# Kernel tuning notes

Measured on AMD Instinct MI355X. Metric: run time of the kernel, lower is better.

## Reference

```python
import jax, jax.numpy as jnp
import numpy as np

D_MODEL = 256
NHEAD = 8
HEAD_DIM = D_MODEL // NHEAD
NLAYERS = 8
LAYER_NAMES = ('self', 'cross', 'self', 'cross', 'self', 'cross', 'self', 'cross')
LN_EPS = 1e-5
ATTN_EPS = 1e-6


def _layernorm(x, g, b):
    mu = jnp.mean(x, axis=-1, keepdims=True)
    var = jnp.mean(jnp.square(x - mu), axis=-1, keepdims=True)
    return (x - mu) * jax.lax.rsqrt(var + LN_EPS) * g + b


def _encoder_layer(x, source, Wq, Wk, Wv, Wm, W1, W2, g1, b1, g2, b2):
    # x: [N, L, C], source: [N, S, C]; weights stored [in, out] so y = x @ W
    bs, L, C = x.shape
    S = source.shape[1]
    q = (x @ Wq).reshape(bs, L, NHEAD, HEAD_DIM)
    k = (source @ Wk).reshape(bs, S, NHEAD, HEAD_DIM)
    v = (source @ Wv).reshape(bs, S, NHEAD, HEAD_DIM)
    # LoFTR LinearAttention: feature map elu(x)+1, O(N d^2) kernelized attention
    Q = jax.nn.elu(q) + 1.0
    K = jax.nn.elu(k) + 1.0
    v_n = v / S  # normalize values by kv length for numerical stability
    KV = jnp.einsum('nshd,nshv->nhdv', K, v_n)            # [N,H,D,D]
    Z = 1.0 / (jnp.einsum('nlhd,nhd->nlh', Q, K.sum(axis=1)) + ATTN_EPS)
    msg = jnp.einsum('nlhd,nhdv,nlh->nlhv', Q, KV, Z) * S  # [N,L,H,D]
    msg = msg.reshape(bs, L, C) @ Wm
    msg = _layernorm(msg, g1, b1)
    h = jnp.concatenate([x, msg], axis=-1)                 # [N,L,2C]
    h = jax.nn.relu(h @ W1) @ W2
    h = _layernorm(h, g2, b2)
    return x + h


def _transformer(feat0, feat1, Wq, Wk, Wv, Wm, W1, W2, g1, b1, g2, b2):
    for i, name in enumerate(LAYER_NAMES):
        p = (Wq[i], Wk[i], Wv[i], Wm[i], W1[i], W2[i], g1[i], b1[i], g2[i], b2[i])
        if name == 'self':
            feat0 = _encoder_layer(feat0, feat0, *p)
            feat1 = _encoder_layer(feat1, feat1, *p)
        else:  # cross
            new0 = _encoder_layer(feat0, feat1, *p)
            feat1 = _encoder_layer(feat1, feat0, *p)
            feat0 = new0
    return feat0, feat1


def setup_inputs() -> dict:
    key = jax.random.key(0)
    ks = jax.random.split(key, 8)
    N, L = 4, 4800
    feat0 = jax.random.normal(ks[0], (N, L, D_MODEL), jnp.float32)
    feat1 = jax.random.normal(ks[1], (N, L, D_MODEL), jnp.float32)
    xav = lambda k, fi, fo: jax.random.normal(k, (NLAYERS, fi, fo), jnp.float32) * float(np.sqrt(2.0 / (fi + fo)))
    Wq = xav(ks[2], D_MODEL, D_MODEL)
    Wk = xav(ks[3], D_MODEL, D_MODEL)
    Wv = xav(ks[4], D_MODEL, D_MODEL)
    Wm = xav(ks[5], D_MODEL, D_MODEL)
    W1 = xav(ks[6], 2 * D_MODEL, 2 * D_MODEL)
    W2 = xav(ks[7], 2 * D_MODEL, D_MODEL)
    g1 = jnp.ones((NLAYERS, D_MODEL), jnp.float32)
    b1 = jnp.zeros((NLAYERS, D_MODEL), jnp.float32)
    g2 = jnp.ones((NLAYERS, D_MODEL), jnp.float32)
    b2 = jnp.zeros((NLAYERS, D_MODEL), jnp.float32)
    return dict(feat0=feat0, feat1=feat1, Wq=Wq, Wk=Wk, Wv=Wv, Wm=Wm,
                W1=W1, W2=W2, g1=g1, b1=b1, g2=g2, b2=b2)


def reference(feat0, feat1, Wq, Wk, Wv, Wm, W1, W2, g1, b1, g2, b2):
    return _transformer(feat0, feat1, Wq, Wk, Wv, Wm, W1, W2, g1, b1, g2, b2)
```

## Files before the change

### kernel.cpp

```cpp
#include <hip/hip_runtime.h>
#include <math.h>

#define RTOT 19200
#define RALL 38400
#define CDIM 256
#define SLEN 4800
#define NB 8
#define NHEAD 8
#define HDIM 32
#define SEG 25
#define SCHUNK 192

typedef __attribute__((ext_vector_type(8))) short short8v;
typedef __attribute__((ext_vector_type(4))) float f32x4;

__device__ __forceinline__ ushort f2b(float f) {
    unsigned u = __float_as_uint(f);
    unsigned r = (u + 0x7FFFu + ((u >> 16) & 1u)) >> 16;
    return (ushort)r;
}
__device__ __forceinline__ float b2f(ushort u) {
    return __uint_as_float(((unsigned)u) << 16);
}

template<int ACT> __device__ __forceinline__ float actf(float v) {
    if (ACT == 1) return v > 0.0f ? v + 1.0f : __expf(v);
    if (ACT == 2) return v > 0.0f ? v : 0.0f;
    return v;
}

__device__ __forceinline__ void gload16(const void* g, void* l) {
    __builtin_amdgcn_global_load_lds((const __attribute__((address_space(1))) void*)g,
                                     (__attribute__((address_space(3))) void*)l, 16, 0, 0);
}

template<int ACT, bool CONCAT, int OMODE>
__global__ __launch_bounds__(256) void gemm_bf16(
    const ushort* __restrict__ A, const ushort* __restrict__ A2, int lda,
    const ushort* __restrict__ Bt,
    ushort* __restrict__ O0, ushort* __restrict__ O1, ushort* __restrict__ O2,
    int N, int K)
{
    __shared__ __align__(16) ushort As[128 * 32];
    __shared__ __align__(16) ushort Bs[128 * 32];
    const int t = threadIdx.x;
    const int wave = t >> 6, lane = t & 63;
    const int bm = blockIdx.y * 128, bn = blockIdx.x * 128;
    const int wr = wave >> 1, wc = wave & 1;
    const int lr = lane & 15, lk = (lane >> 4) * 8;

    const int srow = t >> 2;
    const int sgrp = ((t & 3) * 8) ^ ((srow & 3) * 8);
    const ushort* bAr = A + (size_t)(bm + srow) * lda + sgrp;
    const ushort* bA2r = CONCAT ? (A2 + (size_t)(bm + srow) * lda + sgrp) : (const ushort*)0;
    const ushort* bBr = Bt + (size_t)(bn + srow) * K + sgrp;
    char* ldsA = (char*)As + wave * 1024;
    char* ldsB = (char*)Bs + wave * 1024;
    const size_t a64 = (size_t)64 * lda;
    const size_t b64 = (size_t)64 * K;

    const f32x4 z4 = {0.f, 0.f, 0.f, 0.f};
    f32x4 acc[4][4];
    #pragma unroll
    for (int m = 0; m < 4; ++m)
        #pragma unroll
        for (int n = 0; n < 4; ++n) acc[m][n] = z4;

    for (int k0 = 0; k0 < K; k0 += 32) {
        const ushort* ga;
        if (CONCAT) ga = (k0 < 256) ? (bAr + k0) : (bA2r + (k0 - 256));
        else        ga = bAr + k0;
        gload16(ga, ldsA);
        gload16(ga + a64, ldsA + 4096);
        gload16(bBr + k0, ldsB);
        gload16(bBr + k0 + b64, ldsB + 4096);
        __syncthreads();

        short8v af[4], bfr[4];
        #pragma unroll
        for (int m = 0; m < 4; ++m) {
            const int r = wr * 64 + m * 16 + lr;
            af[m] = *(const short8v*)&As[r * 32 + (lk ^ ((r & 3) * 8))];
        }
        #pragma unroll
        for (int n = 0; n < 4; ++n) {
            const int r = wc * 64 + n * 16 + lr;
            bfr[n] = *(const short8v*)&Bs[r * 32 + (lk ^ ((r & 3) * 8))];
        }
        #pragma unroll
        for (int m = 0; m < 4; ++m)
            #pragma unroll
            for (int n = 0; n < 4; ++n)
                acc[m][n] = __builtin_amdgcn_mfma_f32_16x16x32_bf16(af[m], bfr[n], acc[m][n], 0, 0, 0);
        __syncthreads();
    }

    const int orow = bm + wr * 64 + (lane >> 4) * 4;
    const int ocol = bn + wc * 64 + lr;
    #pragma unroll
    for (int m = 0; m < 4; ++m)
        #pragma unroll
        for (int n = 0; n < 4; ++n)
            #pragma unroll
            for (int j = 0; j < 4; ++j) {
                const float v = acc[m][n][j];
                const size_t row = (size_t)(orow + m * 16 + j);
                const int col = ocol + n * 16;
                if (OMODE == 0) {
                    O0[row * N + col] = f2b(actf<ACT>(v));
                } else {
                    const int seg = col >> 8, c = col & 255;
                    ushort* dst = seg == 0 ? O0 : (seg == 1 ? O1 : O2);
                    dst[row * 256 + c] = f2b(seg < 2 ? actf<1>(v) : v);
                }
            }
}

template<bool RES>
__global__ __launch_bounds__(256) void gemm_ln(
    const ushort* __restrict__ A, int lda,
    const ushort* __restrict__ Bt,
    const float* __restrict__ g, const float* __restrict__ bb,
    const float* __restrict__ rx0, const float* __restrict__ rx1,
    float* __restrict__ outf, ushort* __restrict__ outb, int K)
{
    __shared__ __align__(16) ushort As[64 * 32];
    __shared__ __align__(16) ushort Bs[256 * 32];
    __shared__ float red[2][4][64];
    const int t = threadIdx.x;
    const int wave = t >> 6, lane = t & 63;
    const int bm = blockIdx.x * 64;
    const int lr = lane & 15, kg = lane >> 4, lk = kg * 8;

    const int srow = t >> 2;
    const int sg = ((t & 3) * 8) ^ ((srow & 3) * 8);
    const ushort* aP = A + (size_t)(bm + srow) * lda + sg;
    const ushort* bP = Bt + (size_t)srow * K + sg;
    char* ldsA = (char*)As + wave * 1024;
    char* ldsB = (char*)Bs + wave * 1024;
    const size_t b64 = (size_t)64 * K;

    const f32x4 z4 = {0.f, 0.f, 0.f, 0.f};
    f32x4 acc[4][4];
    #pragma unroll
    for (int m = 0; m < 4; ++m)
        #pragma unroll
        for (int n = 0; n < 4; ++n) acc[m][n] = z4;

    for (int k0 = 0; k0 < K; k0 += 32) {
        gload16(aP + k0, ldsA);
        gload16(bP + k0, ldsB);
        gload16(bP + k0 + b64, ldsB + 4096);
        gload16(bP + k0 + 2 * b64, ldsB + 8192);
        gload16(bP + k0 + 3 * b64, ldsB + 12288);
        __syncthreads();

        short8v af[4], bfr[4];
        #pragma unroll
        for (int m = 0; m < 4; ++m) {
            const int r = m * 16 + lr;
            af[m] = *(const short8v*)&As[r * 32 + (lk ^ ((r & 3) * 8))];
        }
        #pragma unroll
        for (int n = 0; n < 4; ++n) {
            const int r = wave * 64 + n * 16 + lr;
            bfr[n] = *(const short8v*)&Bs[r * 32 + (lk ^ ((r & 3) * 8))];
        }
        #pragma unroll
        for (int m = 0; m < 4; ++m)
            #pragma unroll
            for (int n = 0; n < 4; ++n)
                acc[m][n] = __builtin_amdgcn_mfma_f32_16x16x32_bf16(af[m], bfr[n], acc[m][n], 0, 0, 0);
        __syncthreads();
    }

    #pragma unroll
    for (int m = 0; m < 4; ++m)
        #pragma unroll
        for (int j = 0; j < 4; ++j) {
            float s = 0.f, q = 0.f;
            #pragma unroll
            for (int n = 0; n < 4; ++n) { const float v = acc[m][n][j]; s += v; q += v * v; }
            #pragma unroll
            for (int mk = 1; mk < 16; mk <<= 1) { s += __shfl_xor(s, mk); q += __shfl_xor(q, mk); }
            if (lr == 0) {
                red[0][wave][m * 16 + kg * 4 + j] = s;
                red[1][wave][m * 16 + kg * 4 + j] = q;
            }
        }
    __syncthreads();

    float gv[4], bv[4];
    #pragma unroll
    for (int n = 0; n < 4; ++n) {
        const int col = wave * 64 + n * 16 + lr;
        gv[n] = g[col]; bv[n] = bb[col];
    }
    const float* rxb = (const float*)0;
    if (RES) rxb = (bm < RTOT) ? rx0 + (size_t)bm * CDIM : rx1 + (size_t)(bm - RTOT) * CDIM;

    #pragma unroll
    for (int m = 0; m < 4; ++m)
        #pragma unroll
        for (int j = 0; j < 4; ++j) {
            const int row = m * 16 + kg * 4 + j;
            const float tot = red[0][0][row] + red[0][1][row] + red[0][2][row] + red[0][3][row];
            const float tq  = red[1][0][row] + red[1][1][row] + red[1][2][row] + red[1][3][row];
            const float mu = tot * (1.0f / 256.0f);
            const float var = tq * (1.0f / 256.0f) - mu * mu;
            const float inv = rsqrtf(var + 1e-5f);
            const size_t go = (size_t)(bm + row) * CDIM;
            #pragma unroll
            for (int n = 0; n < 4; ++n) {
                const int col = wave * 64 + n * 16 + lr;
                float val = (acc[m][n][j] - mu) * inv * gv[n] + bv[n];
                if (RES) {
                    val += rxb[(size_t)row * CDIM + col];
                    outf[go + col] = val;
                }
                outb[go + col] = f2b(val);
            }
        }
}

__global__ __launch_bounds__(256) void wconv_t(
    const float* __restrict__ src, ushort* __restrict__ dst, int R, int C, size_t dstride)
{
    __shared__ float tile[32][33];
    const int l = blockIdx.z;
    const int r0 = blockIdx.y * 32, c0 = blockIdx.x * 32;
    const int tx = threadIdx.x & 31, ty = threadIdx.x >> 5;
    const float* s = src + (size_t)l * R * C;
    ushort* d = dst + (size_t)l * dstride;
    for (int i = ty; i < 32; i += 8) tile[i][tx] = s[(size_t)(r0 + i) * C + c0 + tx];
    __syncthreads();
    for (int i = ty; i < 32; i += 8) d[(size_t)(c0 + i) * R + r0 + tx] = f2b(tile[tx][i]);
}

__global__ __launch_bounds__(256) void kv_part_k(
    const ushort* __restrict__ Kb, const ushort* __restrict__ Vb,
    float* __restrict__ KVp, float* __restrict__ Ksp)
{
    const int blk = blockIdx.x;
    const int seg = blk % SEG;
    const int h = (blk / SEG) % NHEAD;
    const int n = blk / (SEG * NHEAD);
    const int s0 = seg * SCHUNK;
    __shared__ float Ks[16][32];
    __shared__ float Vs[16][32];
    const int t = threadIdx.x;
    const int rr = t >> 4, c2 = (t & 15) * 2;
    const int d = t >> 3, v0 = (t & 7) * 4;
    float a0 = 0, a1 = 0, a2 = 0, a3 = 0, ksum = 0;
    for (int c = 0; c < SCHUNK; c += 16) {
        const size_t off = ((size_t)(n * SLEN + s0 + c + rr)) * CDIM + h * HDIM + c2;
        const ushort2 ku = *(const ushort2*)&Kb[off];
        const ushort2 vu = *(const ushort2*)&Vb[off];
        Ks[rr][c2] = b2f(ku.x); Ks[rr][c2 + 1] = b2f(ku.y);
        Vs[rr][c2] = b2f(vu.x); Vs[rr][c2 + 1] = b2f(vu.y);
        __syncthreads();
        #pragma unroll
        for (int q = 0; q < 16; ++q) {
            const float kd = Ks[q][d];
            a0 += kd * Vs[q][v0 + 0];
            a1 += kd * Vs[q][v0 + 1];
            a2 += kd * Vs[q][v0 + 2];
            a3 += kd * Vs[q][v0 + 3];
        }
        if (t < 32) {
            #pragma unroll
            for (int q = 0; q < 16; ++q) ksum += Ks[q][t];
        }
        __syncthreads();
    }
    float* kvp = KVp + ((size_t)((n * NHEAD + h) * SEG + seg)) * 1024;
    kvp[t * 4 + 0] = a0;
    kvp[t * 4 + 1] = a1;
    kvp[t * 4 + 2] = a2;
    kvp[t * 4 + 3] = a3;
    if (t < 32) Ksp[((size_t)((n * NHEAD + h) * SEG + seg)) * 32 + t] = ksum;
}

__global__ __launch_bounds__(256) void kv_reduce_k(
    const float* __restrict__ KVp, const float* __restrict__ Ksp,
    ushort* __restrict__ KVbT, ushort* __restrict__ Ksb)
{
    const int nh = blockIdx.x;
    const int t = threadIdx.x;
    #pragma unroll
    for (int i = 0; i < 4; ++i) {
        const int idx = t * 4 + i;
        const int v = idx >> 5, d = idx & 31;
        float s = 0;
        for (int seg = 0; seg < SEG; ++seg)
            s += KVp[((size_t)(nh * SEG + seg)) * 1024 + d * 32 + v];
        KVbT[(size_t)nh * 1024 + idx] = f2b(s);
    }
    #pragma unroll
    for (int i = 0; i < 2; ++i) {
        const int idx = t * 2 + i;
        const int c = idx >> 5, d = idx & 31;
        float s = 0;
        if (c == 0)
            for (int seg = 0; seg < SEG; ++seg)
                s += Ksp[((size_t)(nh * SEG + seg)) * 32 + d];
        Ksb[(size_t)nh * 512 + idx] = f2b(s);
    }
}

__global__ __launch_bounds__(256) void attn_mfma(
    const ushort* __restrict__ Qb, const ushort* __restrict__ KVbT,
    const ushort* __restrict__ Ksb, ushort* __restrict__ msg, int xorv)
{
    const int n = blockIdx.y;
    const int src = n ^ xorv;
    const int t = threadIdx.x, wave = t >> 6, lane = t & 63;
    const int rw = blockIdx.x * 64 + wave * 16;
    const int lr = lane & 15, kg = lane >> 4;
    const size_t qrow = ((size_t)n * SLEN + rw + lr) * CDIM;
    const f32x4 z4 = {0.f, 0.f, 0.f, 0.f};
    #pragma unroll
    for (int h = 0; h < NHEAD; ++h) {
        const short8v af = *(const short8v*)&Qb[qrow + h * 32 + kg * 8];
        const ushort* bbp = KVbT + ((size_t)(src * NHEAD + h)) * 1024;
        const short8v b0 = *(const short8v*)&bbp[lr * 32 + kg * 8];
        const short8v b1 = *(const short8v*)&bbp[(16 + lr) * 32 + kg * 8];
        const short8v bz = *(const short8v*)&Ksb[((size_t)(src * NHEAD + h)) * 512 + lr * 32 + kg * 8];
        f32x4 a0 = __builtin_amdgcn_mfma_f32_16x16x32_bf16(af, b0, z4, 0, 0, 0);
        f32x4 a1 = __builtin_amdgcn_mfma_f32_16x16x32_bf16(af, b1, z4, 0, 0, 0);
        f32x4 az = __builtin_amdgcn_mfma_f32_16x16x32_bf16(af, bz, z4, 0, 0, 0);
        #pragma unroll
        for (int j = 0; j < 4; ++j) {
            const float zj = __shfl(az[j], lane & 48);
            const float rz = 1.0f / (zj + 1e-6f);
            const size_t orow = ((size_t)n * SLEN + rw + kg * 4 + j) * CDIM + h * 32;
            msg[orow + lr]      = f2b(a0[j] * rz);
            msg[orow + 16 + lr] = f2b(a1[j] * rz);
        }
    }
}

__global__ __launch_bounds__(256) void cvt_in_k(const float* __restrict__ src, ushort* __restrict__ dst) {
    const size_t i = ((size_t)blockIdx.x * 256 + threadIdx.x) * 4;
    const float4 v = *(const float4*)&src[i];
    ushort4 ob = make_ushort4(f2b(v.x), f2b(v.y), f2b(v.z), f2b(v.w));
    *(ushort4*)&dst[i] = ob;
}

struct Ws {
    float *xf, *KVp, *Ksp;
    ushort *xb, *Qb, *Kb, *Vb, *h1b, *KVbT, *Ksb;
    ushort *WqkvT, *WmT, *W1T, *W2T;
};

static void layer_pass(const float* rx0, const float* rx1, float* destf, int xorv,
                       const ushort* WqkvT, const ushort* WmT,
                       const ushort* W1T, const ushort* W2T,
                       const float* g1, const float* b1,
                       const float* g2, const float* b2,
                       const Ws& w, hipStream_t stream)
{
    const dim3 blk(256);
    gemm_bf16<0, false, 1><<<dim3(6, RALL / 128), blk, 0, stream>>>(
        w.xb, nullptr, 256, WqkvT, w.Qb, w.Kb, w.Vb, 768, 256);
    kv_part_k<<<dim3(NB * NHEAD * SEG), blk, 0, stream>>>(w.Kb, w.Vb, w.KVp, w.Ksp);
    kv_reduce_k<<<dim3(NB * NHEAD), blk, 0, stream>>>(w.KVp, w.Ksp, w.KVbT, w.Ksb);
    attn_mfma<<<dim3(SLEN / 64, NB), blk, 0, stream>>>(w.Qb, w.KVbT, w.Ksb, w.Vb, xorv);
    gemm_ln<false><<<dim3(RALL / 64), blk, 0, stream>>>(
        w.Vb, 256, WmT, g1, b1, nullptr, nullptr, nullptr, w.Kb, 256);
    gemm_bf16<2, true, 0><<<dim3(4, RALL / 128), blk, 0, stream>>>(
        w.xb, w.Kb, 256, W1T, w.h1b, nullptr, nullptr, 512, 512);
    gemm_ln<true><<<dim3(RALL / 64), blk, 0, stream>>>(
        w.h1b, 512, W2T, g2, b2, rx0, rx1, destf, w.xb, 512);
}

extern "C" void kernel_launch(void* const* d_in, const int* in_sizes, int n_in,
                              void* d_out, int out_size, void* d_ws, size_t ws_size,
                              hipStream_t stream) {
    (void)in_sizes; (void)n_in; (void)out_size; (void)ws_size;
    const float* f0in = (const float*)d_in[0];
    const float* f1in = (const float*)d_in[1];
    const float* WqA = (const float*)d_in[2];
    const float* WkA = (const float*)d_in[3];
    const float* WvA = (const float*)d_in[4];
    const float* WmA = (const float*)d_in[5];
    const float* W1A = (const float*)d_in[6];
    const float* W2A = (const float*)d_in[7];
    const float* g1A = (const float*)d_in[8];
    const float* b1A = (const float*)d_in[9];
    const float* g2A = (const float*)d_in[10];
    const float* b2A = (const float*)d_in[11];

    float* outf = (float*)d_out;
    const size_t RC = (size_t)RTOT * CDIM;
    const size_t RAC = (size_t)RALL * CDIM;

    float* wsf = (float*)d_ws;
    Ws w;
    w.xf  = wsf;
    w.KVp = w.xf + RAC;
    w.Ksp = w.KVp + (size_t)64 * SEG * 1024;
    ushort* p = (ushort*)(w.Ksp + 64 * SEG * 32);
    w.xb = p;   p += RAC;
    w.Qb = p;   p += RAC;
    w.Kb = p;   p += RAC;
    w.Vb = p;   p += RAC;
    w.h1b = p;  p += (size_t)RALL * 512;
    w.KVbT = p; p += 64 * 1024;
    w.Ksb = p;  p += 64 * 512;
    w.WqkvT = p; p += (size_t)8 * 768 * 256;
    w.WmT = p;  p += (size_t)8 * 256 * 256;
    w.W1T = p;  p += (size_t)8 * 512 * 512;
    w.W2T = p;  p += (size_t)8 * 512 * 256;

    const dim3 blk(256);
    wconv_t<<<dim3(8, 8, 8), blk, 0, stream>>>(WqA, w.WqkvT,             256, 256, 768 * 256);
    wconv_t<<<dim3(8, 8, 8), blk, 0, stream>>>(WkA, w.WqkvT + 256 * 256, 256, 256, 768 * 256);
    wconv_t<<<dim3(8, 8, 8), blk, 0, stream>>>(WvA, w.WqkvT + 512 * 256, 256, 256, 768 * 256);
    wconv_t<<<dim3(8, 8, 8), blk, 0, stream>>>(WmA, w.WmT, 256, 256, 65536);
    wconv_t<<<dim3(16, 16, 8), blk, 0, stream>>>(W1A, w.W1T, 512, 512, 262144);
    wconv_t<<<dim3(8, 16, 8), blk, 0, stream>>>(W2A, w.W2T, 512, 256, 131072);

    cvt_in_k<<<dim3(RC / 1024), blk, 0, stream>>>(f0in, w.xb);
    cvt_in_k<<<dim3(RC / 1024), blk, 0, stream>>>(f1in, w.xb + RC);

    for (int l = 0; l < 8; ++l) {
        const int xorv = (l & 1) ? 4 : 0;
        const float* rx0 = (l == 0) ? f0in : w.xf;
        const float* rx1 = (l == 0) ? f1in : w.xf + RC;
        float* destf = (l == 7) ? outf : w.xf;
        layer_pass(rx0, rx1, destf, xorv,
                   w.WqkvT + (size_t)l * 768 * 256,
                   w.WmT + (size_t)l * 65536,
                   w.W1T + (size_t)l * 262144,
                   w.W2T + (size_t)l * 131072,
                   g1A + l * 256, b1A + l * 256, g2A + l * 256, b2A + l * 256,
                   w, stream);
    }
}
```

Before: 1.600 ms.

## Fuse linear-attention apply with Wm projection and LayerNorm; shrink LN GEMM row tile

The separate attention-apply kernel and the Wm GEMM+LayerNorm kernel are merged into one kernel. Two waves compute the 32-row attention message into swizzled LDS, then all four waves run the Wm GEMM and LayerNorm from that LDS tile. This removes the global write and re-read of the message tensor and one launch per layer. The W2 GEMM+LN kernel also moves from 64-row to 32-row tiles, doubling the block count for occupancy, at the cost of more redundant loads of the weight tile and idle waves during the attention phase.

After: 1.501 ms. -6.2%, faster.

```diff
diff --git a/kernel.cpp b/kernel.cpp
--- a/kernel.cpp
+++ b/kernel.cpp
@@ -116,20 +116,19 @@
             }
 }
 
-template<bool RES>
-__global__ __launch_bounds__(256) void gemm_ln(
+__global__ __launch_bounds__(256) void gemm_ln32(
     const ushort* __restrict__ A, int lda,
     const ushort* __restrict__ Bt,
     const float* __restrict__ g, const float* __restrict__ bb,
     const float* __restrict__ rx0, const float* __restrict__ rx1,
     float* __restrict__ outf, ushort* __restrict__ outb, int K)
 {
-    __shared__ __align__(16) ushort As[64 * 32];
+    __shared__ __align__(16) ushort As[32 * 32];
     __shared__ __align__(16) ushort Bs[256 * 32];
-    __shared__ float red[2][4][64];
+    __shared__ float red[2][4][32];
     const int t = threadIdx.x;
     const int wave = t >> 6, lane = t & 63;
-    const int bm = blockIdx.x * 64;
+    const int bm = blockIdx.x * 32;
     const int lr = lane & 15, kg = lane >> 4, lk = kg * 8;
 
     const int srow = t >> 2;
@@ -141,23 +140,23 @@
     const size_t b64 = (size_t)64 * K;
 
     const f32x4 z4 = {0.f, 0.f, 0.f, 0.f};
-    f32x4 acc[4][4];
-    #pragma unroll
-    for (int m = 0; m < 4; ++m)
+    f32x4 acc[2][4];
+    #pragma unroll
+    for (int m = 0; m < 2; ++m)
         #pragma unroll
         for (int n = 0; n < 4; ++n) acc[m][n] = z4;
 
     for (int k0 = 0; k0 < K; k0 += 32) {
-        gload16(aP + k0, ldsA);
+        if (srow < 32) gload16(aP + k0, ldsA);
         gload16(bP + k0, ldsB);
         gload16(bP + k0 + b64, ldsB + 4096);
         gload16(bP + k0 + 2 * b64, ldsB + 8192);
         gload16(bP + k0 + 3 * b64, ldsB + 12288);
         __syncthreads();
 
-        short8v af[4], bfr[4];
-        #pragma unroll
-        for (int m = 0; m < 4; ++m) {
+        short8v af[2], bfr[4];
+        #pragma unroll
+        for (int m = 0; m < 2; ++m) {
             const int r = m * 16 + lr;
             af[m] = *(const short8v*)&As[r * 32 + (lk ^ ((r & 3) * 8))];
         }
@@ -167,7 +166,7 @@
             bfr[n] = *(const short8v*)&Bs[r * 32 + (lk ^ ((r & 3) * 8))];
         }
         #pragma unroll
-        for (int m = 0; m < 4; ++m)
+        for (int m = 0; m < 2; ++m)
             #pragma unroll
             for (int n = 0; n < 4; ++n)
                 acc[m][n] = __builtin_amdgcn_mfma_f32_16x16x32_bf16(af[m], bfr[n], acc[m][n], 0, 0, 0);
@@ -175,7 +174,7 @@
     }
 
     #pragma unroll
-    for (int m = 0; m < 4; ++m)
+    for (int m = 0; m < 2; ++m)
         #pragma unroll
         for (int j = 0; j < 4; ++j) {
             float s = 0.f, q = 0.f;
@@ -196,11 +195,10 @@
         const int col = wave * 64 + n * 16 + lr;
         gv[n] = g[col]; bv[n] = bb[col];
     }
-    const float* rxb = (const float*)0;
-    if (RES) rxb = (bm < RTOT) ? rx0 + (size_t)bm * CDIM : rx1 + (size_t)(bm - RTOT) * CDIM;
-
-    #pragma unroll
-    for (int m = 0; m < 4; ++m)
+    const float* rxb = (bm < RTOT) ? rx0 + (size_t)bm * CDIM : rx1 + (size_t)(bm - RTOT) * CDIM;
+
+    #pragma unroll
+    for (int m = 0; m < 2; ++m)
         #pragma unroll
         for (int j = 0; j < 4; ++j) {
             const int row = m * 16 + kg * 4 + j;
@@ -214,11 +212,129 @@
             for (int n = 0; n < 4; ++n) {
                 const int col = wave * 64 + n * 16 + lr;
                 float val = (acc[m][n][j] - mu) * inv * gv[n] + bv[n];
-                if (RES) {
-                    val += rxb[(size_t)row * CDIM + col];
-                    outf[go + col] = val;
-                }
+                val += rxb[(size_t)row * CDIM + col];
+                outf[go + col] = val;
                 outb[go + col] = f2b(val);
+            }
+        }
+}
+
+__global__ __launch_bounds__(256) void attn_wm_ln(
+    const ushort* __restrict__ Qb, const ushort* __restrict__ KVbT,
+    const ushort* __restrict__ Ksb, const ushort* __restrict__ WmT,
+    const float* __restrict__ g, const float* __restrict__ bb,
+    ushort* __restrict__ mln, int xorv)
+{
+    __shared__ __align__(16) ushort Ms[32 * 256];
+    __shared__ __align__(16) ushort Bs[256 * 32];
+    __shared__ float red[2][4][32];
+    const int t = threadIdx.x, wave = t >> 6, lane = t & 63;
+    const int bm = blockIdx.x * 32;
+    const int n = bm / SLEN, src = n ^ xorv;
+    const int lr = lane & 15, kg = lane >> 4, lk = kg * 8;
+    const f32x4 z4 = {0.f, 0.f, 0.f, 0.f};
+
+    if (wave < 2) {
+        const int rw = wave * 16;
+        const size_t qrow = ((size_t)bm + rw + lr) * CDIM;
+        char* mb = (char*)Ms;
+        #pragma unroll
+        for (int h = 0; h < NHEAD; ++h) {
+            const short8v af = *(const short8v*)&Qb[qrow + h * 32 + kg * 8];
+            const ushort* bbp = KVbT + ((size_t)(src * NHEAD + h)) * 1024;
+            const short8v b0 = *(const short8v*)&bbp[lr * 32 + kg * 8];
+            const short8v b1 = *(const short8v*)&bbp[(16 + lr) * 32 + kg * 8];
+            const short8v bz = *(const short8v*)&Ksb[((size_t)(src * NHEAD + h)) * 512 + lr * 32 + kg * 8];
+            f32x4 a0 = __builtin_amdgcn_mfma_f32_16x16x32_bf16(af, b0, z4, 0, 0, 0);
+            f32x4 a1 = __builtin_amdgcn_mfma_f32_16x16x32_bf16(af, b1, z4, 0, 0, 0);
+            f32x4 az = __builtin_amdgcn_mfma_f32_16x16x32_bf16(af, bz, z4, 0, 0, 0);
+            #pragma unroll
+            for (int j = 0; j < 4; ++j) {
+                const float zj = __shfl(az[j], lane & 48);
+                const float rz = 1.0f / (zj + 1e-6f);
+                const int orow = rw + kg * 4 + j;
+                const int swz = (orow & 7) << 4;
+                *(ushort*)(mb + ((orow * 512 + (h * 32 + lr) * 2) ^ swz)) = f2b(a0[j] * rz);
+                *(ushort*)(mb + ((orow * 512 + (h * 32 + 16 + lr) * 2) ^ swz)) = f2b(a1[j] * rz);
+            }
+        }
+    }
+    __syncthreads();
+
+    const int srow = t >> 2;
+    const int sg = ((t & 3) * 8) ^ ((srow & 3) * 8);
+    const ushort* bP = WmT + (size_t)srow * 256 + sg;
+    char* ldsB = (char*)Bs + wave * 1024;
+
+    f32x4 acc[2][4];
+    #pragma unroll
+    for (int m = 0; m < 2; ++m)
+        #pragma unroll
+        for (int nn = 0; nn < 4; ++nn) acc[m][nn] = z4;
+
+    for (int k0 = 0; k0 < 256; k0 += 32) {
+        gload16(bP + k0, ldsB);
+        gload16(bP + k0 + 64 * 256, ldsB + 4096);
+        gload16(bP + k0 + 128 * 256, ldsB + 8192);
+        gload16(bP + k0 + 192 * 256, ldsB + 12288);
+        __syncthreads();
+
+        short8v af[2], bfr[4];
+        #pragma unroll
+        for (int m = 0; m < 2; ++m) {
+            const int r = m * 16 + lr;
+            af[m] = *(const short8v*)((char*)Ms + ((r * 512 + k0 * 2 + kg * 16) ^ ((r & 7) << 4)));
+        }
+        #pragma unroll
+        for (int nn = 0; nn < 4; ++nn) {
+            const int r = wave * 64 + nn * 16 + lr;
+            bfr[nn] = *(const short8v*)&Bs[r * 32 + (lk ^ ((r & 3) * 8))];
+        }
+        #pragma unroll
+        for (int m = 0; m < 2; ++m)
+            #pragma unroll
+            for (int nn = 0; nn < 4; ++nn)
+                acc[m][nn] = __builtin_amdgcn_mfma_f32_16x16x32_bf16(af[m], bfr[nn], acc[m][nn], 0, 0, 0);
+        __syncthreads();
+    }
+
+    #pragma unroll
+    for (int m = 0; m < 2; ++m)
+        #pragma unroll
+        for (int j = 0; j < 4; ++j) {
+            float s = 0.f, q = 0.f;
+            #pragma unroll
+            for (int nn = 0; nn < 4; ++nn) { const float v = acc[m][nn][j]; s += v; q += v * v; }
+            #pragma unroll
+            for (int mk = 1; mk < 16; mk <<= 1) { s += __shfl_xor(s, mk); q += __shfl_xor(q, mk); }
+            if (lr == 0) {
+                red[0][wave][m * 16 + kg * 4 + j] = s;
+                red[1][wave][m * 16 + kg * 4 + j] = q;
+            }
+        }
+    __syncthreads();
+
+    float gv[4], bv[4];
+    #pragma unroll
+    for (int nn = 0; nn < 4; ++nn) {
+        const int col = wave * 64 + nn * 16 + lr;
+        gv[nn] = g[col]; bv[nn] = bb[col];
+    }
+    #pragma unroll
+    for (int m = 0; m < 2; ++m)
+        #pragma unroll
+        for (int j = 0; j < 4; ++j) {
+            const int row = m * 16 + kg * 4 + j;
+            const float tot = red[0][0][row] + red[0][1][row] + red[0][2][row] + red[0][3][row];
+            const float tq  = red[1][0][row] + red[1][1][row] + red[1][2][row] + red[1][3][row];
+            const float mu = tot * (1.0f / 256.0f);
+            const float var = tq * (1.0f / 256.0f) - mu * mu;
+            const float inv = rsqrtf(var + 1e-5f);
+            const size_t go = (size_t)(bm + row) * CDIM;
+            #pragma unroll
+            for (int nn = 0; nn < 4; ++nn) {
+                const int col = wave * 64 + nn * 16 + lr;
+                mln[go + col] = f2b((acc[m][nn][j] - mu) * inv * gv[nn] + bv[nn]);
             }
         }
 }
@@ -308,38 +424,6 @@
     }
 }
 
-__global__ __launch_bounds__(256) void attn_mfma(
-    const ushort* __restrict__ Qb, const ushort* __restrict__ KVbT,
-    const ushort* __restrict__ Ksb, ushort* __restrict__ msg, int xorv)
-{
-    const int n = blockIdx.y;
-    const int src = n ^ xorv;
-    const int t = threadIdx.x, wave = t >> 6, lane = t & 63;
-    const int rw = blockIdx.x * 64 + wave * 16;
-    const int lr = lane & 15, kg = lane >> 4;
-    const size_t qrow = ((size_t)n * SLEN + rw + lr) * CDIM;
-    const f32x4 z4 = {0.f, 0.f, 0.f, 0.f};
-    #pragma unroll
-    for (int h = 0; h < NHEAD; ++h) {
-        const short8v af = *(const short8v*)&Qb[qrow + h * 32 + kg * 8];
-        const ushort* bbp = KVbT + ((size_t)(src * NHEAD + h)) * 1024;
-        const short8v b0 = *(const short8v*)&bbp[lr * 32 + kg * 8];
-        const short8v b1 = *(const short8v*)&bbp[(16 + lr) * 32 + kg * 8];
-        const short8v bz = *(const short8v*)&Ksb[((size_t)(src * NHEAD + h)) * 512 + lr * 32 + kg * 8];
-        f32x4 a0 = __builtin_amdgcn_mfma_f32_16x16x32_bf16(af, b0, z4, 0, 0, 0);
-        f32x4 a1 = __builtin_amdgcn_mfma_f32_16x16x32_bf16(af, b1, z4, 0, 0, 0);
-        f32x4 az = __builtin_amdgcn_mfma_f32_16x16x32_bf16(af, bz, z4, 0, 0, 0);
-        #pragma unroll
-        for (int j = 0; j < 4; ++j) {
-            const float zj = __shfl(az[j], lane & 48);
-            const float rz = 1.0f / (zj + 1e-6f);
-            const size_t orow = ((size_t)n * SLEN + rw + kg * 4 + j) * CDIM + h * 32;
-            msg[orow + lr]      = f2b(a0[j] * rz);
-            msg[orow + 16 + lr] = f2b(a1[j] * rz);
-        }
-    }
-}
-
 __global__ __launch_bounds__(256) void cvt_in_k(const float* __restrict__ src, ushort* __restrict__ dst) {
     const size_t i = ((size_t)blockIdx.x * 256 + threadIdx.x) * 4;
     const float4 v = *(const float4*)&src[i];
@@ -365,12 +449,11 @@
         w.xb, nullptr, 256, WqkvT, w.Qb, w.Kb, w.Vb, 768, 256);
     kv_part_k<<<dim3(NB * NHEAD * SEG), blk, 0, stream>>>(w.Kb, w.Vb, w.KVp, w.Ksp);
     kv_reduce_k<<<dim3(NB * NHEAD), blk, 0, stream>>>(w.KVp, w.Ksp, w.KVbT, w.Ksb);
-    attn_mfma<<<dim3(SLEN / 64, NB), blk, 0, stream>>>(w.Qb, w.KVbT, w.Ksb, w.Vb, xorv);
-    gemm_ln<false><<<dim3(RALL / 64), blk, 0, stream>>>(
-        w.Vb, 256, WmT, g1, b1, nullptr, nullptr, nullptr, w.Kb, 256);
+    attn_wm_ln<<<dim3(RALL / 32), blk, 0, stream>>>(
+        w.Qb, w.KVbT, w.Ksb, WmT, g1, b1, w.Kb, xorv);
     gemm_bf16<2, true, 0><<<dim3(4, RALL / 128), blk, 0, stream>>>(
         w.xb, w.Kb, 256, W1T, w.h1b, nullptr, nullptr, 512, 512);
-    gemm_ln<true><<<dim3(RALL / 64), blk, 0, stream>>>(
+    gemm_ln32<<<dim3(RALL / 32), blk, 0, stream>>>(
         w.h1b, 512, W2T, g2, b2, rx0, rx1, destf, w.xb, 512);
 }
 
```
